# Kernel tuning notes

Measured on AMD Instinct MI355X. Metric: run time of the kernel, lower is better.

Reference implementation:

```python
import jax, jax.numpy as jnp
from jax import lax
import numpy as np

N, L, E, NHEAD, DFF = 16, 1024, 512, 8, 2048
HD = E // NHEAD
NLEVELS = 10  # log2(1024)
S_SCALES = NLEVELS + 1


def setup_inputs() -> dict:
    key = jax.random.key(0)
    ks = jax.random.split(key, 12)
    s = 0.05
    return {
        "src": jax.random.normal(ks[0], (N, L, E), jnp.float32),
        "conv_w": jax.random.normal(ks[1], (NLEVELS, HD, HD, 2), jnp.float32) * s,
        "conv_b": jax.random.normal(ks[2], (NLEVELS, HD), jnp.float32) * s,
        "in_proj_w": jax.random.normal(ks[3], (3 * E, E), jnp.float32) * s,
        "in_proj_b": jax.random.normal(ks[4], (3 * E,), jnp.float32) * s,
        "out_proj_w": jax.random.normal(ks[5], (E, E), jnp.float32) * s,
        "out_proj_b": jax.random.normal(ks[6], (E,), jnp.float32) * s,
        "ln1_w": jnp.ones((E,), jnp.float32),
        "ln1_b": jnp.zeros((E,), jnp.float32),
        "ln2_w": jnp.ones((E,), jnp.float32),
        "ln2_b": jnp.zeros((E,), jnp.float32),
        "w1": jax.random.normal(ks[7], (DFF, E), jnp.float32) * s,
        "b1": jax.random.normal(ks[8], (DFF,), jnp.float32) * s,
        "w2": jax.random.normal(ks[9], (E, DFF), jnp.float32) * s,
        "b2": jax.random.normal(ks[10], (E,), jnp.float32) * s,
    }


def _layer_norm(x, w, b, eps=1e-5):
    mu = jnp.mean(x, axis=-1, keepdims=True)
    var = jnp.mean(jnp.square(x - mu), axis=-1, keepdims=True)
    return (x - mu) * lax.rsqrt(var + eps) * w + b


def _forward(src, conv_w, conv_b, in_proj_w, in_proj_b, out_proj_w, out_proj_b,
             ln1_w, ln1_b, ln2_w, ln2_b, w1, b1, w2, b2):
    n, l, e = src.shape
    hd = e // NHEAD
    # pyramid over 1D spatial dim, channels-first
    out = jnp.transpose(src, (0, 2, 1))  # (N, E, L)
    hidden_vals = [out]
    for i in range(NLEVELS):
        x = out.reshape(n * NHEAD, hd, out.shape[-1])  # (N*H, hd, li)
        x = lax.conv_general_dilated(
            x, conv_w[i], window_strides=(2,), padding='VALID',
            dimension_numbers=('NCH', 'OIH', 'NCH'))
        x = jax.nn.relu(x + conv_b[i][None, :, None])
        out = x.reshape(n, e, x.shape[-1])  # (N, E, li/2)
        # upsample back to full length via repeat_interleave
        hidden_vals.append(jnp.repeat(out, l // out.shape[-1], axis=2))
    hv = jnp.stack(hidden_vals, -1)                      # (N, E, L, S)
    s = hv.shape[-1]
    hv = jnp.transpose(hv, (3, 0, 2, 1)).reshape(s, n * l, e)  # (S, N*L, E)

    # multi-head attention: length-1 query (finest scale) over all scales
    b_ = n * l
    q = hv[0:1] @ in_proj_w[:e].T + in_proj_b[:e]            # (1, B, E)
    k = hv @ in_proj_w[e:2 * e].T + in_proj_b[e:2 * e]       # (S, B, E)
    v = hv @ in_proj_w[2 * e:].T + in_proj_b[2 * e:]         # (S, B, E)
    qh = jnp.transpose(q.reshape(1, b_, NHEAD, hd), (1, 2, 0, 3))  # (B, H, 1, hd)
    kh = jnp.transpose(k.reshape(s, b_, NHEAD, hd), (1, 2, 0, 3))  # (B, H, S, hd)
    vh = jnp.transpose(v.reshape(s, b_, NHEAD, hd), (1, 2, 0, 3))  # (B, H, S, hd)
    scores = jnp.einsum('bhqd,bhkd->bhqk', qh, kh) / jnp.sqrt(jnp.float32(hd))
    attn = jax.nn.softmax(scores, axis=-1)
    o = jnp.einsum('bhqk,bhkd->bhqd', attn, vh)              # (B, H, 1, hd)
    o = o.reshape(b_, e) @ out_proj_w.T + out_proj_b         # (B, E)
    src2 = o.reshape(n, l, e)

    # faithful to source: residual computed then overwritten by norm1(src2)
    x = _layer_norm(src2, ln1_w, ln1_b)
    ff = jax.nn.relu(x @ w1.T + b1) @ w2.T + b2
    return _layer_norm(x + ff, ln2_w, ln2_b)


def reference(src, conv_w, conv_b, in_proj_w, in_proj_b, out_proj_w, out_proj_b,
              ln1_w, ln1_b, ln2_w, ln2_b, w1, b1, w2, b2):
    return _forward(src, conv_w, conv_b, in_proj_w, in_proj_b, out_proj_w,
                    out_proj_b, ln1_w, ln1_b, ln2_w, ln2_b, w1, b1, w2, b2)
```

## Files before the change

kernel.cpp:

```cpp
#include <hip/hip_runtime.h>
#include <hip/hip_bf16.h>
#include <stdint.h>
#include <math.h>

#define NB      16
#define LL      1024
#define EE      512
#define NHEADS  8
#define DFF     2048
#define NLEVELS 10
#define NSCALES 11
#define BROWS   (NB * LL)

typedef unsigned short u16;
typedef __attribute__((ext_vector_type(8))) short bf16x8;
typedef __attribute__((ext_vector_type(4))) float f32x4;

static const size_t B_SRCBF = 0;
static const size_t B_LVLBF = 16777216;
static const size_t B_QKV   = 33538048;
static const size_t B_KVS   = 83869696;
static const size_t B_OBF   = 117391360;
static const size_t B_XPRE  = 134168576;
static const size_t B_OUTBF = 150945792;
static const size_t B_XBF   = 167723008;
static const size_t B_WBF   = 184500224;
static const size_t B_FFH   = 0;

__device__ __forceinline__ u16 f2bf(float x) {
    union { float f; uint32_t u; } c; c.f = x;
    uint32_t u = c.u + 0x7FFFu + ((c.u >> 16) & 1u);
    return (u16)(u >> 16);
}
__device__ __forceinline__ float bf2f(u16 v) {
    union { uint32_t u; float f; } c; c.u = ((uint32_t)v) << 16; return c.f;
}
__device__ __forceinline__ uint32_t addbf2(uint32_t a, uint32_t b) {
    float lo = bf2f((u16)(a & 0xFFFF)) + bf2f((u16)(b & 0xFFFF));
    float hi = bf2f((u16)(a >> 16))    + bf2f((u16)(b >> 16));
    return (uint32_t)f2bf(lo) | ((uint32_t)f2bf(hi) << 16);
}
__device__ __forceinline__ void ld8bf(const u16* p, float* f) {
    uint4 r = *(const uint4*)p;
    uint32_t ws[4] = { r.x, r.y, r.z, r.w };
    #pragma unroll
    for (int j = 0; j < 4; j++) {
        union { uint32_t u; float g; } lo, hi;
        lo.u = ws[j] << 16; hi.u = ws[j] & 0xFFFF0000u;
        f[2 * j] = lo.g; f[2 * j + 1] = hi.g;
    }
}
__device__ __forceinline__ void gload16(const u16* g, u16* l) {
    __builtin_amdgcn_global_load_lds(
        (const __attribute__((address_space(1))) void*)g,
        (__attribute__((address_space(3))) void*)l, 16, 0, 0);
}

__global__ void cast_all_kernel(const float* __restrict__ s0, const float* __restrict__ s1,
                                const float* __restrict__ s2, const float* __restrict__ s3,
                                const float* __restrict__ s4, const float* __restrict__ cw,
                                u16* __restrict__ d0, u16* __restrict__ d1,
                                u16* __restrict__ d2, u16* __restrict__ d3,
                                u16* __restrict__ d4, u16* __restrict__ dw)
{
    int bid = blockIdx.x;
    if (bid >= 11264) {
        int base = (bid - 11264) * 1024 + threadIdx.x * 4;
        #pragma unroll
        for (int j = 0; j < 4; j++) {
            int idx = base + j;
            int lvl = idx >> 13, rem = idx & 8191;
            int o = rem >> 7, ck = rem & 127;
            int k = ck >> 6, ci = ck & 63;
            dw[idx] = f2bf(cw[(lvl << 13) + (o << 7) + (ci << 1) + k]);
        }
        return;
    }
    const float* s; u16* d; int nt;
    if      (bid < 8192)  { s = s0; d = d0; nt = 2097152; }
    else if (bid < 8960)  { bid -= 8192;  s = s1; d = d1; nt = 196608; }
    else if (bid < 9216)  { bid -= 8960;  s = s2; d = d2; nt = 65536;  }
    else if (bid < 10240) { bid -= 9216;  s = s3; d = d3; nt = 262144; }
    else                  { bid -= 10240; s = s4; d = d4; nt = 262144; }
    int i = bid * 256 + threadIdx.x;
    if (i < nt) {
        float4 v = ((const float4*)s)[i];
        uint2 o;
        o.x = (uint32_t)f2bf(v.x) | ((uint32_t)f2bf(v.y) << 16);
        o.y = (uint32_t)f2bf(v.z) | ((uint32_t)f2bf(v.w) << 16);
        ((uint2*)d)[i] = o;
    }
}

__global__ __launch_bounds__(256, 2)
void conv_chain_kernel(const u16* __restrict__ src_bf, u16* __restrict__ lvl_bf,
                       const u16* __restrict__ cw, const float* __restrict__ cb)
{
    __shared__ u16 BIG[16384];
    __shared__ u16 MID[8192];
    __shared__ u16 WB[8192];
    const int tid = threadIdx.x;
    const int l = tid & 63, w = tid >> 6;
    const int bid = blockIdx.x;
    const int q  = bid & 3;
    const int h  = (bid >> 2) & 7;
    const int n  = bid >> 5;

    {
        const u16* base = src_bf + ((size_t)n * 1024 + q * 256) * 512 + h * 64;
        #pragma unroll
        for (int j = 0; j < 8; j++) {
            int c = j * 256 + w * 64 + l;
            int row = c >> 3, lch = c & 7;
            int gch = lch ^ (row & 7);
            gload16(base + (size_t)row * 512 + gch * 8,
                    BIG + (size_t)(j * 256 + w * 64) * 8);
        }
    }

    const u16* IN = BIG;
    u16* OUTb = MID;
    int R = 128;
    int T = 512;
    size_t rowOff = 0;
    for (int lvl = 1; lvl <= 8; lvl++) {
        {
            const u16* wsrc = cw + (size_t)(lvl - 1) * 8192;
            #pragma unroll
            for (int j = 0; j < 4; j++) {
                int c = j * 256 + w * 64 + l;
                int o = c >> 4, lch = c & 15;
                int gch = lch ^ (o & 7);
                gload16(wsrc + o * 128 + gch * 8, WB + (size_t)(j * 256 + w * 64) * 8);
            }
        }
        asm volatile("s_waitcnt vmcnt(0)" ::: "memory");
        __syncthreads();

        const int nrt = (R + 15) >> 4;
        const int maxil = 2 * R - 1;
        for (int f = w; f < nrt * 4; f += 4) {
            int rt = f >> 2, nc = f & 3;
            int o = nc * 16 + (l & 15);
            f32x4 acc = {0.f, 0.f, 0.f, 0.f};
            #pragma unroll
            for (int s = 0; s < 4; s++) {
                int il = 2 * (rt * 16 + (l & 15)) + (s >> 1);
                if (il > maxil) il = maxil;
                int ach = (((s & 1) * 4) + (l >> 4)) ^ (il & 7);
                bf16x8 av = *(const bf16x8*)(IN + il * 64 + ach * 8);
                int bch = (s * 4 + (l >> 4)) ^ (o & 7);
                bf16x8 bv = *(const bf16x8*)(WB + o * 128 + bch * 8);
                acc = __builtin_amdgcn_mfma_f32_16x16x32_bf16(av, bv, acc, 0, 0, 0);
            }
            float bb = cb[(lvl - 1) * 64 + o];
            #pragma unroll
            for (int reg = 0; reg < 4; reg++) {
                int rloc = rt * 16 + (l >> 4) * 4 + reg;
                if (rloc < R) {
                    float v = fmaxf(acc[reg] + bb, 0.f);
                    u16 b16 = f2bf(v);
                    lvl_bf[(rowOff + (size_t)n * T + (size_t)q * R + rloc) * 512 + h * 64 + o] = b16;
                    OUTb[rloc * 64 + (((o >> 3) ^ (rloc & 7)) << 3) + (o & 7)] = b16;
                }
            }
        }
        __syncthreads();
        const u16* tmp = IN; IN = OUTb; OUTb = (u16*)tmp;
        rowOff += (size_t)16 * T;
        T >>= 1; R >>= 1;
    }
}

__global__ void conv_tail_kernel(u16* __restrict__ lvl_bf, const u16* __restrict__ cw,
                                 const float* __restrict__ cb)
{
    const int h = blockIdx.x & 7, n = blockIdx.x >> 3;
    const int tid = threadIdx.x;
    __shared__ float L8s[4][64];
    __shared__ float L9s[2][64];
    {
        int r = tid >> 6, c = tid & 63;
        L8s[r][c] = bf2f(lvl_bf[((size_t)16256 + n * 4 + r) * 512 + h * 64 + c]);
    }
    __syncthreads();
    if (tid < 128) {
        int t = tid >> 6, o = tid & 63;
        const u16* wr = cw + (size_t)8 * 8192 + o * 128;
        float acc = cb[8 * 64 + o];
        #pragma unroll
        for (int k = 0; k < 2; k++)
            #pragma unroll 16
            for (int ci = 0; ci < 64; ci++)
                acc += L8s[2 * t + k][ci] * bf2f(wr[k * 64 + ci]);
        acc = fmaxf(acc, 0.f);
        L9s[t][o] = acc;
        lvl_bf[((size_t)16320 + n * 2 + t) * 512 + h * 64 + o] = f2bf(acc);
    }
    __syncthreads();
    if (tid < 64) {
        int o = tid;
        const u16* wr = cw + (size_t)9 * 8192 + o * 128;
        float acc = cb[9 * 64 + o];
        #pragma unroll
        for (int k = 0; k < 2; k++)
            #pragma unroll 16
            for (int ci = 0; ci < 64; ci++)
                acc += L9s[k][ci] * bf2f(wr[k * 64 + ci]);
        acc = fmaxf(acc, 0.f);
        lvl_bf[((size_t)16352 + n) * 512 + h * 64 + o] = f2bf(acc);
    }
}

__device__ __forceinline__ void gemm_v4_body(
    u16* lds,
    const u16* __restrict__ A, const u16* __restrict__ W,
    const float* __restrict__ bias, const u16* __restrict__ resb,
    u16* __restrict__ Cb, int M, int K, int N, int relu, int gx,
    int nwg, int bid)
{
    const int tid = threadIdx.x;
    const int l = tid & 63, w = tid >> 6;
    const int wm = w >> 1, wn = w & 1;

    const int q = nwg >> 3, r = nwg & 7;
    const int xcd = bid & 7, idx = bid >> 3;
    const int lin = (xcd < r ? xcd * (q + 1) : r * (q + 1) + (xcd - r) * q) + idx;
    const int by = lin / gx, bx = lin - by * gx;
    const int rowBase = by * 256, colBase = bx * 128;

    f32x4 acc[4][4];
    #pragma unroll
    for (int m = 0; m < 4; m++)
        #pragma unroll
        for (int n = 0; n < 4; n++) acc[m][n] = 0.f;

    const u16* gApt[2];
    const u16* gBpt;
    #pragma unroll
    for (int i = 0; i < 2; i++) {
        int G = i * 512 + tid;
        int row = G >> 2, p = G & 3;
        int c = p ^ ((row >> 1) & 3);
        int grow = rowBase + row; if (grow > M - 1) grow = M - 1;
        gApt[i] = A + (size_t)grow * K + c * 8;
    }
    {
        int G = tid;
        int row = G >> 2, p = G & 3;
        int c = p ^ ((row >> 1) & 3);
        gBpt = W + (size_t)(colBase + row) * K + c * 8;
    }

    const int NT = K >> 5;
    auto STAGE = [&](int tt, int buf) {
        const int kb = tt << 5;
        u16* dA = lds + buf * 12288;
        u16* dB = dA + 8192;
        gload16(gApt[0] + kb, dA + (size_t)(w * 64) * 8);
        gload16(gApt[1] + kb, dA + (size_t)(512 + w * 64) * 8);
        gload16(gBpt + kb, dB + (size_t)(w * 64) * 8);
    };
    STAGE(0, 0);
    if (NT > 1) STAGE(1, 1);

    int cbuf = 0, sbuf = 2;
    for (int t = 0; t < NT; ++t) {
        if (t + 1 < NT) asm volatile("s_waitcnt vmcnt(3)" ::: "memory");
        else            asm volatile("s_waitcnt vmcnt(0)" ::: "memory");
        __builtin_amdgcn_s_barrier();
        __builtin_amdgcn_sched_barrier(0);
        if (t + 2 < NT) STAGE(t + 2, sbuf);

        const u16* Ab = lds + cbuf * 12288;
        const u16* Bb = Ab + 8192;
        const int c = l >> 4;
        bf16x8 av[4], bv[4];
        #pragma unroll
        for (int fr = 0; fr < 4; fr++) {
            int row = wm * 64 + fr * 16 + (l & 15);
            av[fr] = *(const bf16x8*)(Ab + row * 32 + ((c ^ ((row >> 1) & 3)) * 8));
        }
        #pragma unroll
        for (int fc = 0; fc < 4; fc++) {
            int col = wn * 64 + fc * 16 + (l & 15);
            bv[fc] = *(const bf16x8*)(Bb + col * 32 + ((c ^ ((col >> 1) & 3)) * 8));
        }
        __builtin_amdgcn_s_setprio(1);
        #pragma unroll
        for (int m = 0; m < 4; m++)
            #pragma unroll
            for (int n = 0; n < 4; n++)
                acc[m][n] = __builtin_amdgcn_mfma_f32_16x16x32_bf16(av[m], bv[n], acc[m][n], 0, 0, 0);
        __builtin_amdgcn_s_setprio(0);

        cbuf = (cbuf == 2) ? 0 : cbuf + 1;
        sbuf = (sbuf == 2) ? 0 : sbuf + 1;
    }
    __builtin_amdgcn_s_barrier();
    __builtin_amdgcn_sched_barrier(0);

    const int cc = colBase + wn * 64 + (l & 15);
    float bs4[4];
    #pragma unroll
    for (int n = 0; n < 4; n++) bs4[n] = bias[cc + n * 16];

    u16* WS = lds + w * 2048;
    #pragma unroll
    for (int hh = 0; hh < 2; hh++) {
        #pragma unroll
        for (int mi = 0; mi < 2; mi++) {
            #pragma unroll
            for (int n = 0; n < 4; n++) {
                int colv = n * 16 + (l & 15);
                #pragma unroll
                for (int reg = 0; reg < 4; reg++) {
                    int rowh = mi * 16 + (l >> 4) * 4 + reg;
                    float v = acc[hh * 2 + mi][n][reg] + bs4[n];
                    if (relu) v = fmaxf(v, 0.f);
                    WS[rowh * 64 + (colv ^ (((rowh >> 2) & 3) << 4))] = f2bf(v);
                }
            }
        }
        asm volatile("s_waitcnt lgkmcnt(0)" ::: "memory");
        __builtin_amdgcn_sched_barrier(0);
        #pragma unroll
        for (int j = 0; j < 4; j++) {
            int rowh = (l >> 3) + 8 * j;
            int col8 = (l & 7) * 8;
            int colx = col8 ^ (((rowh >> 2) & 3) << 4);
            uint4 v = *(const uint4*)(WS + rowh * 64 + colx);
            int grow = rowBase + wm * 64 + hh * 32 + rowh;
            if (grow < M) {
                int gcol = colBase + wn * 64 + col8;
                if (resb) {
                    uint4 rb = *(const uint4*)&resb[(size_t)grow * N + gcol];
                    v.x = addbf2(v.x, rb.x);
                    v.y = addbf2(v.y, rb.y);
                    v.z = addbf2(v.z, rb.z);
                    v.w = addbf2(v.w, rb.w);
                }
                *(uint4*)(Cb + (size_t)grow * N + gcol) = v;
            }
        }
        asm volatile("s_waitcnt lgkmcnt(0)" ::: "memory");
    }
}

__global__ __launch_bounds__(512, 4)
void mfma_gemm(const u16* __restrict__ A, const u16* __restrict__ W,
               const float* __restrict__ bias, const u16* __restrict__ resb,
               u16* __restrict__ Cb, int M, int K, int N, int relu, int gx)
{
    __shared__ u16 lds[36864];
    gemm_v4_body(lds, A, W, bias, resb, Cb, M, K, N, relu, gx,
                 gridDim.x, blockIdx.x);
}

__global__ __launch_bounds__(512, 4)
void mfma_gemm_dual(const u16* __restrict__ A0, const u16* __restrict__ W0,
                    const float* __restrict__ b0, u16* __restrict__ C0,
                    int M0, int K0, int N0, int gx0, int n0,
                    const u16* __restrict__ A1, const u16* __restrict__ W1,
                    const float* __restrict__ b1, u16* __restrict__ C1,
                    int M1, int K1, int N1, int gx1, int n1)
{
    __shared__ u16 lds[36864];
    if ((int)blockIdx.x < n0)
        gemm_v4_body(lds, A0, W0, b0, nullptr, C0, M0, K0, N0, 0, gx0,
                     n0, blockIdx.x);
    else
        gemm_v4_body(lds, A1, W1, b1, nullptr, C1, M1, K1, N1, 0, gx1,
                     n1, blockIdx.x - n0);
}

__global__ void attn_kernel(const u16* __restrict__ QKV, const u16* __restrict__ KVs,
                            u16* __restrict__ O)
{
    const int wv   = threadIdx.x >> 6;
    const int lane = threadIdx.x & 63;
    const int bswz = (blockIdx.x & 7) * (gridDim.x >> 3) + (blockIdx.x >> 3);
    const int b    = bswz * 4 + wv;
    const int h    = lane >> 3;
    const int d8   = lane & 7;
    const int n = b >> 10, pos = b & 1023;

    float q[8];
    ld8bf(QKV + (size_t)b * 1536 + h * 64 + d8 * 8, q);

    float sc[NSCALES];
    {
        float kk[8];
        ld8bf(QKV + (size_t)b * 1536 + 512 + h * 64 + d8 * 8, kk);
        float p = 0.f;
        #pragma unroll
        for (int j = 0; j < 8; j++) p += q[j] * kk[j];
        p += __shfl_xor(p, 1); p += __shfl_xor(p, 2); p += __shfl_xor(p, 4);
        sc[0] = p * 0.125f;
    }
    {
        int rowOff = 0;
        #pragma unroll
        for (int s = 1; s <= NLEVELS; s++) {
            int Ls = 1024 >> s;
            int row = rowOff + n * Ls + (pos >> s);
            float kk[8];
            ld8bf(KVs + (size_t)row * 1024 + h * 64 + d8 * 8, kk);
            float p = 0.f;
            #pragma unroll
            for (int j = 0; j < 8; j++) p += q[j] * kk[j];
            p += __shfl_xor(p, 1); p += __shfl_xor(p, 2); p += __shfl_xor(p, 4);
            sc[s] = p * 0.125f;
            rowOff += 16 * Ls;
        }
    }
    float m = sc[0];
    #pragma unroll
    for (int s = 1; s < NSCALES; s++) m = fmaxf(m, sc[s]);
    float sum = 0.f;
    #pragma unroll
    for (int s = 0; s < NSCALES; s++) { sc[s] = __expf(sc[s] - m); sum += sc[s]; }
    float inv = 1.f / sum;

    float o[8] = {};
    {
        float vv[8];
        ld8bf(QKV + (size_t)b * 1536 + 1024 + h * 64 + d8 * 8, vv);
        float a = sc[0] * inv;
        #pragma unroll
        for (int j = 0; j < 8; j++) o[j] += a * vv[j];
    }
    {
        int rowOff = 0;
        #pragma unroll
        for (int s = 1; s <= NLEVELS; s++) {
            int Ls = 1024 >> s;
            int row = rowOff + n * Ls + (pos >> s);
            float vv[8];
            ld8bf(KVs + (size_t)row * 1024 + 512 + h * 64 + d8 * 8, vv);
            float a = sc[s] * inv;
            #pragma unroll
            for (int j = 0; j < 8; j++) o[j] += a * vv[j];
            rowOff += 16 * Ls;
        }
    }
    uint4 pk;
    pk.x = (uint32_t)f2bf(o[0]) | ((uint32_t)f2bf(o[1]) << 16);
    pk.y = (uint32_t)f2bf(o[2]) | ((uint32_t)f2bf(o[3]) << 16);
    pk.z = (uint32_t)f2bf(o[4]) | ((uint32_t)f2bf(o[5]) << 16);
    pk.w = (uint32_t)f2bf(o[6]) | ((uint32_t)f2bf(o[7]) << 16);
    *(uint4*)(O + (size_t)b * 512 + h * 64 + d8 * 8) = pk;
}

__global__ void ln_bf_kernel(const u16* __restrict__ in_bf,
                             const float* __restrict__ w, const float* __restrict__ b,
                             u16* __restrict__ out_bf, float* __restrict__ out_f)
{
    const int l = threadIdx.x & 63;
    const int row = blockIdx.x * 4 + (threadIdx.x >> 6);
    float v[8];
    ld8bf(in_bf + (size_t)row * EE + l * 8, v);
    float s = 0.f, s2 = 0.f;
    #pragma unroll
    for (int j = 0; j < 8; j++) { s += v[j]; s2 += v[j] * v[j]; }
    #pragma unroll
    for (int m = 1; m < 64; m <<= 1) { s += __shfl_xor(s, m); s2 += __shfl_xor(s2, m); }
    float mu  = s * (1.f / 512.f);
    float var = s2 * (1.f / 512.f) - mu * mu;
    float rs  = rsqrtf(var + 1e-5f);
    float4 w0 = *(const float4*)&w[l * 8], w1 = *(const float4*)&w[l * 8 + 4];
    float4 b0 = *(const float4*)&b[l * 8], b1 = *(const float4*)&b[l * 8 + 4];
    float o[8];
    o[0] = (v[0] - mu) * rs * w0.x + b0.x;
    o[1] = (v[1] - mu) * rs * w0.y + b0.y;
    o[2] = (v[2] - mu) * rs * w0.z + b0.z;
    o[3] = (v[3] - mu) * rs * w0.w + b0.w;
    o[4] = (v[4] - mu) * rs * w1.x + b1.x;
    o[5] = (v[5] - mu) * rs * w1.y + b1.y;
    o[6] = (v[6] - mu) * rs * w1.z + b1.z;
    o[7] = (v[7] - mu) * rs * w1.w + b1.w;
    if (out_bf) {
        uint4 pk;
        pk.x = (uint32_t)f2bf(o[0]) | ((uint32_t)f2bf(o[1]) << 16);
        pk.y = (uint32_t)f2bf(o[2]) | ((uint32_t)f2bf(o[3]) << 16);
        pk.z = (uint32_t)f2bf(o[4]) | ((uint32_t)f2bf(o[5]) << 16);
        pk.w = (uint32_t)f2bf(o[6]) | ((uint32_t)f2bf(o[7]) << 16);
        *(uint4*)(out_bf + (size_t)row * EE + l * 8) = pk;
    }
    if (out_f) {
        float* po = out_f + (size_t)row * EE + l * 8;
        *(float4*)po       = make_float4(o[0], o[1], o[2], o[3]);
        *(float4*)(po + 4) = make_float4(o[4], o[5], o[6], o[7]);
    }
}

extern "C" void kernel_launch(void* const* d_in, const int* in_sizes, int n_in,
                              void* d_out, int out_size, void* d_ws, size_t ws_size,
                              hipStream_t stream)
{
    const float* src        = (const float*)d_in[0];
    const float* conv_w     = (const float*)d_in[1];
    const float* conv_b     = (const float*)d_in[2];
    const float* in_proj_w  = (const float*)d_in[3];
    const float* in_proj_b  = (const float*)d_in[4];
    const float* out_proj_w = (const float*)d_in[5];
    const float* out_proj_b = (const float*)d_in[6];
    const float* ln1_w      = (const float*)d_in[7];
    const float* ln1_b      = (const float*)d_in[8];
    const float* ln2_w      = (const float*)d_in[9];
    const float* ln2_b      = (const float*)d_in[10];
    const float* w1         = (const float*)d_in[11];
    const float* b1         = (const float*)d_in[12];
    const float* w2         = (const float*)d_in[13];
    const float* b2         = (const float*)d_in[14];

    char*  wsb    = (char*)d_ws;
    float* out    = (float*)d_out;
    u16*   src_bf = (u16*)(wsb + B_SRCBF);
    u16*   lvl_bf = (u16*)(wsb + B_LVLBF);
    u16*   QKV    = (u16*)(wsb + B_QKV);
    u16*   KVs    = (u16*)(wsb + B_KVS);
    u16*   O_bf   = (u16*)(wsb + B_OBF);
    u16*   XPRE   = (u16*)(wsb + B_XPRE);
    u16*   OUTBF  = (u16*)(wsb + B_OUTBF);
    u16*   X_bf   = (u16*)(wsb + B_XBF);
    u16*   inw_bf = (u16*)(wsb + B_WBF);
    u16*   outw_bf= inw_bf + 786432;
    u16*   w1_bf  = outw_bf + 262144;
    u16*   w2_bf  = w1_bf + 1048576;
    u16*   cw_bf  = w2_bf + 1048576;
    u16*   FFH    = (u16*)(wsb + B_FFH);

    cast_all_kernel<<<11344, 256, 0, stream>>>(src, in_proj_w, out_proj_w, w1, w2, conv_w,
                                               src_bf, inw_bf, outw_bf, w1_bf, w2_bf, cw_bf);

    conv_chain_kernel<<<NB * NHEADS * 4, 256, 0, stream>>>(src_bf, lvl_bf, cw_bf, conv_b);
    conv_tail_kernel<<<NB * NHEADS, 256, 0, stream>>>(lvl_bf, cw_bf, conv_b);

    mfma_gemm_dual<<<768 + 512, 512, 0, stream>>>(
        src_bf, inw_bf, in_proj_b, QKV, BROWS, EE, 1536, 12, 768,
        lvl_bf, inw_bf + (size_t)512 * 512, in_proj_b + 512, KVs,
        16368, EE, 1024, 8, 512);

    attn_kernel<<<BROWS / 4, 256, 0, stream>>>(QKV, KVs, O_bf);

    mfma_gemm<<<64 * 4, 512, 0, stream>>>(
        O_bf, outw_bf, out_proj_b, nullptr, XPRE, BROWS, EE, EE, 0, 4);

    ln_bf_kernel<<<BROWS / 4, 256, 0, stream>>>(XPRE, ln1_w, ln1_b, X_bf, nullptr);

    mfma_gemm<<<64 * 16, 512, 0, stream>>>(
        X_bf, w1_bf, b1, nullptr, FFH, BROWS, EE, DFF, 1, 16);

    mfma_gemm<<<64 * 4, 512, 0, stream>>>(
        FFH, w2_bf, b2, X_bf, OUTBF, BROWS, DFF, EE, 0, 4);

    ln_bf_kernel<<<BROWS / 4, 256, 0, stream>>>(OUTBF, ln2_w, ln2_b, nullptr, out);
}
```

Before: 226.0 us.

## Co-schedule conv pyramid chain with query-projection GEMM in one launch

```diff
diff --git a/kernel.cpp b/kernel.cpp
--- a/kernel.cpp
+++ b/kernel.cpp
@@ -92,16 +92,15 @@
     }
 }
 
-__global__ __launch_bounds__(256, 2)
-void conv_chain_kernel(const u16* __restrict__ src_bf, u16* __restrict__ lvl_bf,
-                       const u16* __restrict__ cw, const float* __restrict__ cb)
-{
-    __shared__ u16 BIG[16384];
-    __shared__ u16 MID[8192];
-    __shared__ u16 WB[8192];
+__device__ __forceinline__ void conv_chain_body(
+    u16* lds, const u16* __restrict__ src_bf, u16* __restrict__ lvl_bf,
+    const u16* __restrict__ cw, const float* __restrict__ cb, int bid)
+{
+    u16* BIG = lds;
+    u16* MID = lds + 16384;
+    u16* WB  = lds + 24576;
     const int tid = threadIdx.x;
     const int l = tid & 63, w = tid >> 6;
-    const int bid = blockIdx.x;
     const int q  = bid & 3;
     const int h  = (bid >> 2) & 7;
     const int n  = bid >> 5;
@@ -109,12 +108,12 @@
     {
         const u16* base = src_bf + ((size_t)n * 1024 + q * 256) * 512 + h * 64;
         #pragma unroll
-        for (int j = 0; j < 8; j++) {
-            int c = j * 256 + w * 64 + l;
+        for (int j = 0; j < 4; j++) {
+            int c = j * 512 + w * 64 + l;
             int row = c >> 3, lch = c & 7;
             int gch = lch ^ (row & 7);
             gload16(base + (size_t)row * 512 + gch * 8,
-                    BIG + (size_t)(j * 256 + w * 64) * 8);
+                    BIG + (size_t)(j * 512 + w * 64) * 8);
         }
     }
 
@@ -127,11 +126,11 @@
         {
             const u16* wsrc = cw + (size_t)(lvl - 1) * 8192;
             #pragma unroll
-            for (int j = 0; j < 4; j++) {
-                int c = j * 256 + w * 64 + l;
+            for (int j = 0; j < 2; j++) {
+                int c = j * 512 + w * 64 + l;
                 int o = c >> 4, lch = c & 15;
                 int gch = lch ^ (o & 7);
-                gload16(wsrc + o * 128 + gch * 8, WB + (size_t)(j * 256 + w * 64) * 8);
+                gload16(wsrc + o * 128 + gch * 8, WB + (size_t)(j * 512 + w * 64) * 8);
             }
         }
         asm volatile("s_waitcnt vmcnt(0)" ::: "memory");
@@ -139,7 +138,7 @@
 
         const int nrt = (R + 15) >> 4;
         const int maxil = 2 * R - 1;
-        for (int f = w; f < nrt * 4; f += 4) {
+        for (int f = w; f < nrt * 4; f += 8) {
             int rt = f >> 2, nc = f & 3;
             int o = nc * 16 + (l & 15);
             f32x4 acc = {0.f, 0.f, 0.f, 0.f};
@@ -358,20 +357,17 @@
 }
 
 __global__ __launch_bounds__(512, 4)
-void mfma_gemm_dual(const u16* __restrict__ A0, const u16* __restrict__ W0,
-                    const float* __restrict__ b0, u16* __restrict__ C0,
-                    int M0, int K0, int N0, int gx0, int n0,
-                    const u16* __restrict__ A1, const u16* __restrict__ W1,
-                    const float* __restrict__ b1, u16* __restrict__ C1,
-                    int M1, int K1, int N1, int gx1, int n1)
+void conv_qkv_dual(const u16* __restrict__ src_bf, u16* __restrict__ lvl_bf,
+                   const u16* __restrict__ cw, const float* __restrict__ cb,
+                   const u16* __restrict__ inw, const float* __restrict__ inb,
+                   u16* __restrict__ QKV)
 {
     __shared__ u16 lds[36864];
-    if ((int)blockIdx.x < n0)
-        gemm_v4_body(lds, A0, W0, b0, nullptr, C0, M0, K0, N0, 0, gx0,
-                     n0, blockIdx.x);
+    if ((int)blockIdx.x < 512)
+        conv_chain_body(lds, src_bf, lvl_bf, cw, cb, blockIdx.x);
     else
-        gemm_v4_body(lds, A1, W1, b1, nullptr, C1, M1, K1, N1, 0, gx1,
-                     n1, blockIdx.x - n0);
+        gemm_v4_body(lds, src_bf, inw, inb, nullptr, QKV, BROWS, EE, 1536, 0, 12,
+                     768, blockIdx.x - 512);
 }
 
 __global__ void attn_kernel(const u16* __restrict__ QKV, const u16* __restrict__ KVs,
@@ -534,13 +530,14 @@
     cast_all_kernel<<<11344, 256, 0, stream>>>(src, in_proj_w, out_proj_w, w1, w2, conv_w,
                                                src_bf, inw_bf, outw_bf, w1_bf, w2_bf, cw_bf);
 
-    conv_chain_kernel<<<NB * NHEADS * 4, 256, 0, stream>>>(src_bf, lvl_bf, cw_bf, conv_b);
+    conv_qkv_dual<<<512 + 768, 512, 0, stream>>>(
+        src_bf, lvl_bf, cw_bf, conv_b, inw_bf, in_proj_b, QKV);
+
     conv_tail_kernel<<<NB * NHEADS, 256, 0, stream>>>(lvl_bf, cw_bf, conv_b);
 
-    mfma_gemm_dual<<<768 + 512, 512, 0, stream>>>(
-        src_bf, inw_bf, in_proj_b, QKV, BROWS, EE, 1536, 12, 768,
-        lvl_bf, inw_bf + (size_t)512 * 512, in_proj_b + 512, KVs,
-        16368, EE, 1024, 8, 512);
+    mfma_gemm<<<64 * 8, 512, 0, stream>>>(
+        lvl_bf, inw_bf + (size_t)512 * 512, in_proj_b + 512, nullptr, KVs,
+        16368, EE, 1024, 0, 8);
 
     attn_kernel<<<BROWS / 4, 256, 0, stream>>>(QKV, KVs, O_bf);
 
```

Result: no change. 228.0 us (+0.9%).
